# Performance work log

Measured on AMD Instinct MI355X. Metric: run time of the kernel, lower is better.

Reference implementation:

```python
import jax, jax.numpy as jnp
import numpy as np

HID = 256

def lstm_cell(x, h, c, Wih, Whh, bih, bhh):
    # PyTorch LSTM gate order: i, f, g, o
    g = x @ Wih.T + h @ Whh.T + bih + bhh
    i, f, gg, o = jnp.split(g, 4, axis=-1)
    c = jax.nn.sigmoid(f) * c + jax.nn.sigmoid(i) * jnp.tanh(gg)
    h = jax.nn.sigmoid(o) * jnp.tanh(c)
    return h, c

def lstm_seq(x, Wih, Whh, bih, bhh):
    # x: [B, T, D] -> outputs [B, T, H], final (h, c)
    B = x.shape[0]
    h0 = jnp.zeros((B, HID), x.dtype)
    def step(carry, xt):
        h, c = lstm_cell(xt, carry[0], carry[1], Wih, Whh, bih, bhh)
        return (h, c), h
    (h, c), ys = jax.lax.scan(step, (h0, h0), jnp.swapaxes(x, 0, 1))
    return jnp.swapaxes(ys, 0, 1), h, c

def setup_inputs():
    key = jax.random.key(0)
    B, M, H_WIN, NTH, NTW = 512, 16, 25, 64, 64
    SAL = NTH * NTW
    ks = iter(jax.random.split(key, 40))
    def U(shape):
        return jax.random.uniform(next(ks), shape, jnp.float32, -0.0625, 0.0625)
    def lstm_p(pfx, din):
        return {pfx + '_Wih': U((4 * HID, din)), pfx + '_Whh': U((4 * HID, HID)),
                pfx + '_bih': U((4 * HID,)), pfx + '_bhh': U((4 * HID,))}
    inp = {
        'encoder_position_inputs': jax.random.normal(next(ks), (B, M, 3), jnp.float32) * 0.1,
        'encoder_saliency_inputs': jax.random.uniform(next(ks), (B, M, NTH, NTW), jnp.float32),
        'decoder_position_inputs': jax.random.normal(next(ks), (B, 1, 3), jnp.float32) * 0.1,
        'decoder_saliency_inputs': jax.random.uniform(next(ks), (B, H_WIN, NTH, NTW), jnp.float32),
    }
    for pfx, din in [('pe', 3), ('se', SAL), ('fe', 2 * HID), ('pd', 3), ('sd', SAL), ('fd', 2 * HID)]:
        inp.update(lstm_p(pfx, din))
    inp['f2_W'] = U((HID, HID)); inp['f2_b'] = U((HID,))
    inp['out_W'] = U((3, HID)); inp['out_b'] = U((3,))
    return inp

def reference(encoder_position_inputs, encoder_saliency_inputs, decoder_position_inputs, decoder_saliency_inputs,
              pe_Wih, pe_Whh, pe_bih, pe_bhh, se_Wih, se_Whh, se_bih, se_bhh,
              fe_Wih, fe_Whh, fe_bih, fe_bhh, pd_Wih, pd_Whh, pd_bih, pd_bhh,
              sd_Wih, sd_Whh, sd_bih, sd_bhh, fd_Wih, fd_Whh, fd_bih, fd_bhh,
              f2_W, f2_b, out_W, out_b):
    B, M = encoder_position_inputs.shape[:2]
    SAL = encoder_saliency_inputs.shape[2] * encoder_saliency_inputs.shape[3]
    # encoder
    out_pos, h1, c1 = lstm_seq(encoder_position_inputs, pe_Wih, pe_Whh, pe_bih, pe_bhh)
    out_sal, h2, c2 = lstm_seq(encoder_saliency_inputs.reshape(B, M, SAL), se_Wih, se_Whh, se_bih, se_bhh)
    conc_enc = jnp.concatenate([out_sal, out_pos], axis=-1)
    _, hf, cf = lstm_seq(conc_enc, fe_Wih, fe_Whh, fe_bih, fe_bhh)
    # decoder: H_WINDOW single-step recurrence; fuse LSTM restarts from (hf, cf) every step
    dec_sal = decoder_saliency_inputs.reshape(B, -1, SAL)
    def step(carry, sal_t):
        inp, h1, c1, h2, c2 = carry
        h1, c1 = lstm_cell(inp, h1, c1, pd_Wih, pd_Whh, pd_bih, pd_bhh)
        h2, c2 = lstm_cell(sal_t, h2, c2, sd_Wih, sd_Whh, sd_bih, sd_bhh)
        conc = jnp.concatenate([h2, h1], axis=-1)
        hfd, _ = lstm_cell(conc, hf, cf, fd_Wih, fd_Whh, fd_bih, fd_bhh)
        fuse2 = hfd @ f2_W.T + f2_b
        delta = fuse2 @ out_W.T + out_b
        pred = inp + delta  # toPosition: orientation + motion
        return (pred, h1, c1, h2, c2), pred
    init = (decoder_position_inputs[:, 0], h1, c1, h2, c2)
    _, preds = jax.lax.scan(step, init, jnp.swapaxes(dec_sal, 0, 1))
    return jnp.swapaxes(preds, 0, 1)  # [B, H_WINDOW, 3]
```

## Files before the change

### kernel.cpp

```cpp
#include <hip/hip_runtime.h>

#define HID 256
#define BATCH 512
#define MENC 16
#define HWIN 25
#define SALSZ 4096
#define BH (BATCH * HID)

typedef __attribute__((ext_vector_type(8))) short bf16x8;
typedef __attribute__((ext_vector_type(4))) float f32x4;

__device__ __forceinline__ float sigmf(float x) { return 1.0f / (1.0f + __expf(-x)); }
__device__ __forceinline__ ushort f2bf(float f) {
    uint32_t u = __float_as_uint(f);
    return (ushort)((u + 0x7fffu + ((u >> 16) & 1u)) >> 16);
}

#define GLOAD_LDS(gp, lp) \
    __builtin_amdgcn_global_load_lds((const __attribute__((address_space(1))) void*)(gp), \
                                     (__attribute__((address_space(3))) void*)(lp), 16, 0, 0)

__device__ __forceinline__ void st_u64(void* p, unsigned long long v) {
    __hip_atomic_store((unsigned long long*)p, v, __ATOMIC_RELAXED, __HIP_MEMORY_SCOPE_AGENT);
}

__device__ __forceinline__ void gbar_arrive(unsigned int* slot)
{
    __syncthreads();
    if (threadIdx.x == 0) atomicAdd(slot, 1u);
}
__device__ __forceinline__ void gbar_wait(unsigned int* slot, unsigned int nblk)
{
    if (threadIdx.x == 0) {
        while (__hip_atomic_load(slot, __ATOMIC_RELAXED, __HIP_MEMORY_SCOPE_AGENT) < nblk)
            __builtin_amdgcn_s_sleep(1);
    }
    __syncthreads();
}

__device__ __forceinline__ void stage_wtile(const ushort* Wsrc, int ldw, int u0,
                                            ushort* lds, int lane, int wq)
{
    const int sub = lane >> 5, uu = lane & 31;
#pragma unroll
    for (int i = 0; i < 8; ++i) {
        const int row = i * 8 + wq * 2 + sub;
        const int su  = uu ^ (row & 7);
        const int gr  = (row >> 4) * HID + u0 + (row & 15);
        GLOAD_LDS(Wsrc + (size_t)gr * ldw + su * 8, lds + i * 2048 + wq * 512);
    }
}

__device__ __forceinline__ void cell_g(const ushort* hrow0, int ldh,
                                       const ushort* WsL, f32x4 acc[4], int lane)
{
    const int fr = lane & 15, fq = lane >> 4;
    const ushort* hrow = hrow0 + (size_t)fr * ldh;
#pragma unroll
    for (int ks = 0; ks < 8; ++ks) {
        const bf16x8 af = *(const bf16x8*)(hrow + ks * 32 + fq * 8);
#pragma unroll
        for (int g = 0; g < 4; ++g) {
            const int vr = g * 16 + fr;
            const bf16x8 bf = *(const bf16x8*)(WsL + vr * 256 + (((ks * 4 + fq)) ^ (vr & 7)) * 8);
            acc[g] = __builtin_amdgcn_mfma_f32_16x16x32_bf16(af, bf, acc[g], 0, 0, 0);
        }
    }
}

struct Cvt9 {
    const float* s[9];
    ushort*      d[9];
    int          end[9];
};
__global__ __launch_bounds__(256)
void cvt_multi(Cvt9 A)
{
    int i = blockIdx.x * 256 + threadIdx.x;
    if (i >= A.end[8]) return;
    int seg = 0, beg = 0;
#pragma unroll
    for (int k = 0; k < 8; ++k)
        if (i >= A.end[k]) { seg = k + 1; beg = A.end[k]; }
    const int j = i - beg;
    const float4 v = *(const float4*)(A.s[seg] + (size_t)j * 4);
    *(ushort4*)(A.d[seg] + (size_t)j * 4) = make_ushort4(f2bf(v.x), f2bf(v.y), f2bf(v.z), f2bf(v.w));
}

__device__ __forceinline__ void loadA128(const float* Ag, int lda, int tid, float4 ra[4])
{
#pragma unroll
    for (int j = 0; j < 2; ++j) {
        const int idx = j * 512 + tid;
        const int row = idx >> 3, u = idx & 7;
        const int su = (u ^ (row & 7)) * 8;
        ra[2 * j + 0] = *(const float4*)(Ag + (size_t)row * lda + su);
        ra[2 * j + 1] = *(const float4*)(Ag + (size_t)row * lda + su + 4);
    }
}
__device__ __forceinline__ void writeA128(const float4 ra[4], ushort* Al, int tid)
{
#pragma unroll
    for (int j = 0; j < 2; ++j) {
        const int idx = j * 512 + tid;
        uint4 v;
        v.x = (uint)f2bf(ra[2 * j].x) | ((uint)f2bf(ra[2 * j].y) << 16);
        v.y = (uint)f2bf(ra[2 * j].z) | ((uint)f2bf(ra[2 * j].w) << 16);
        v.z = (uint)f2bf(ra[2 * j + 1].x) | ((uint)f2bf(ra[2 * j + 1].y) << 16);
        v.w = (uint)f2bf(ra[2 * j + 1].z) | ((uint)f2bf(ra[2 * j + 1].w) << 16);
        *(uint4*)(Al + idx * 8) = v;
    }
}
__device__ __forceinline__ void stageB128(const ushort* Bg, int ldw, ushort* Bl, int tid)
{
#pragma unroll
    for (int j = 0; j < 2; ++j) {
        const int idx = j * 512 + tid;
        const int row = idx >> 3, u = idx & 7;
        const int su = (u ^ (row & 7)) * 8;
        GLOAD_LDS(Bg + (size_t)row * ldw + su, Bl + idx * 8);
    }
}

__global__ __launch_bounds__(512, 4)
void gemm128f(const float* __restrict__ A, const ushort* __restrict__ W,
              float* __restrict__ C, int M, int N, int K,
              int lda, int ldw, int ldc)
{
    __shared__ ushort As[2][128 * 64];
    __shared__ ushort Bs[2][128 * 64];
    const int tid = threadIdx.x, lane = tid & 63, wid = tid >> 6;

    const int gx = gridDim.x, nwg = gx * gridDim.y;
    int bid = blockIdx.y * gx + blockIdx.x;
    {
        const int q = nwg >> 3, r = nwg & 7;
        const int xcd = bid & 7, o = bid >> 3;
        bid = (xcd < r) ? xcd * (q + 1) + o : r * (q + 1) + (xcd - r) * q + o;
    }
    const int m0 = (bid / gx) * 128, n0 = (bid % gx) * 128;

    const int wr = wid >> 1, wc = wid & 1;
    const int fr = lane & 15, fq = lane >> 4;

    f32x4 acc[2][4] = {};
    const int nt = K / 64;
    const float*  Ab0 = A + (size_t)m0 * lda;
    const ushort* Bb0 = W + (size_t)n0 * ldw;

    float4 ra[4];
    loadA128(Ab0, lda, tid, ra);
    stageB128(Bb0, ldw, Bs[0], tid);
    writeA128(ra, As[0], tid);
    loadA128(Ab0 + 64, lda, tid, ra);
    asm volatile("s_waitcnt vmcnt(4) lgkmcnt(0)" ::: "memory");
    __builtin_amdgcn_sched_barrier(0);
    __builtin_amdgcn_s_barrier();
    __builtin_amdgcn_sched_barrier(0);

    for (int t = 0; t < nt; ++t) {
        const int p = t & 1;
        const int t1 = (t + 1 < nt) ? t + 1 : nt - 1;
        const int t2 = (t + 2 < nt) ? t + 2 : nt - 1;
        stageB128(Bb0 + t1 * 64, ldw, Bs[p ^ 1], tid);
        writeA128(ra, As[p ^ 1], tid);
        loadA128(Ab0 + t2 * 64, lda, tid, ra);

        const ushort* Ab = As[p];
        const ushort* Bb = Bs[p];
#pragma unroll
        for (int ks = 0; ks < 2; ++ks) {
            bf16x8 bfr[4];
#pragma unroll
            for (int nf = 0; nf < 4; ++nf) {
                const int row = wc * 64 + nf * 16 + fr;
                bfr[nf] = *(const bf16x8*)(Bb + row * 64 + ((ks * 4 + fq) ^ (row & 7)) * 8);
            }
            bf16x8 af[2];
#pragma unroll
            for (int mf = 0; mf < 2; ++mf) {
                const int row = wr * 32 + mf * 16 + fr;
                af[mf] = *(const bf16x8*)(Ab + row * 64 + ((ks * 4 + fq) ^ (row & 7)) * 8);
            }
            __builtin_amdgcn_s_setprio(1);
#pragma unroll
            for (int mf = 0; mf < 2; ++mf)
#pragma unroll
                for (int nf = 0; nf < 4; ++nf)
                    acc[mf][nf] = __builtin_amdgcn_mfma_f32_16x16x32_bf16(
                        af[mf], bfr[nf], acc[mf][nf], 0, 0, 0);
            __builtin_amdgcn_s_setprio(0);
        }
        if (t == nt - 1) break;
        asm volatile("s_waitcnt vmcnt(4) lgkmcnt(0)" ::: "memory");
        __builtin_amdgcn_sched_barrier(0);
        __builtin_amdgcn_s_barrier();
        __builtin_amdgcn_sched_barrier(0);
    }

    const int cl = lane & 15, ch = lane >> 4;
#pragma unroll
    for (int mf = 0; mf < 2; ++mf)
#pragma unroll
        for (int nf = 0; nf < 4; ++nf)
#pragma unroll
            for (int r = 0; r < 4; ++r)
                C[(size_t)(m0 + wr * 32 + mf * 16 + ch * 4 + r) * ldc
                  + n0 + wc * 64 + nf * 16 + cl] = acc[mf][nf][r];
}

__global__ __launch_bounds__(256)
void gemm_mfma_bt(const ushort* __restrict__ A, const ushort* __restrict__ W,
                  float* __restrict__ C, int M, int N, int K,
                  int lda, int ldw, int ldc, const float* __restrict__ rbias)
{
    __shared__ ushort As[128 * 32];
    __shared__ ushort Bs[128 * 32];
    const int t    = threadIdx.x;
    const int lane = t & 63, wid = t >> 6;
    const int m0 = blockIdx.y * 128, n0 = blockIdx.x * 128;
    const int wr = wid >> 1, wc = wid & 1;

    f32x4 acc[4][4] = {};

    const int sr = wid * 16 + (lane >> 2);
    const int su = ((lane & 3) ^ ((lane >> 3) & 3)) * 8;
    const ushort* Ag = A + (size_t)(m0 + sr) * lda + su;
    const ushort* Wg = W + (size_t)(n0 + sr) * ldw + su;
    ushort* Al = As + wid * 512;
    ushort* Bl = Bs + wid * 512;

    const int fr = lane & 15;
    const int fq = lane >> 4;
    const int sw = (fr >> 1) & 3;

    for (int k0 = 0; k0 < K; k0 += 32) {
        GLOAD_LDS(Ag,                    Al);
        GLOAD_LDS(Ag + (size_t)64 * lda, Al + 2048);
        GLOAD_LDS(Wg,                    Bl);
        GLOAD_LDS(Wg + (size_t)64 * ldw, Bl + 2048);
        Ag += 32; Wg += 32;
        __syncthreads();

        bf16x8 af[4], bfr[4];
#pragma unroll
        for (int m = 0; m < 4; ++m)
            af[m] = *(const bf16x8*)(As + (wr * 64 + m * 16 + fr) * 32 + (fq ^ sw) * 8);
#pragma unroll
        for (int n = 0; n < 4; ++n)
            bfr[n] = *(const bf16x8*)(Bs + (wc * 64 + n * 16 + fr) * 32 + (fq ^ sw) * 8);
#pragma unroll
        for (int m = 0; m < 4; ++m)
#pragma unroll
            for (int n = 0; n < 4; ++n)
                acc[m][n] = __builtin_amdgcn_mfma_f32_16x16x32_bf16(af[m], bfr[n], acc[m][n], 0, 0, 0);
        __syncthreads();
    }

    const int cl = lane & 15, ch = lane >> 4;
#pragma unroll
    for (int m = 0; m < 4; ++m)
#pragma unroll
        for (int n = 0; n < 4; ++n)
#pragma unroll
            for (int r = 0; r < 4; ++r) {
                const int mm = m0 + wr * 64 + m * 16 + ch * 4 + r;
                const int nn = n0 + wc * 64 + n * 16 + cl;
                float v = acc[m][n][r];
                if (rbias) v += rbias[(size_t)(mm & 511) * ldc + nn];
                C[(size_t)mm * ldc + nn] = v;
            }
}

__global__ __launch_bounds__(256)
void gemm_tn(const float* __restrict__ A, const float* __restrict__ W,
             const float* __restrict__ b1, const float* __restrict__ b2,
             float* __restrict__ C,
             int M, int N, int K, int lda, int ldw, int ldc)
{
    __shared__ float AsT[16][68];
    __shared__ float WsT[16][68];
    const int t  = threadIdx.x;
    const int tx = t & 15, ty = t >> 4;
    const int m0 = blockIdx.y * 64, n0 = blockIdx.x * 64;
    const int lr = t >> 2;
    const int c4 = t & 3;

    float acc[4][4];
#pragma unroll
    for (int i = 0; i < 4; ++i)
#pragma unroll
        for (int j = 0; j < 4; ++j) acc[i][j] = 0.0f;

    for (int k0 = 0; k0 < K; k0 += 16) {
        float a[4], w[4];
        const int kb = k0 + c4 * 4;
#pragma unroll
        for (int k = 0; k < 4; ++k) {
            a[k] = (kb + k < K) ? A[(size_t)(m0 + lr) * lda + kb + k] : 0.0f;
            w[k] = (kb + k < K) ? W[(size_t)(n0 + lr) * ldw + kb + k] : 0.0f;
        }
        __syncthreads();
#pragma unroll
        for (int k = 0; k < 4; ++k) {
            AsT[c4 * 4 + k][lr] = a[k];
            WsT[c4 * 4 + k][lr] = w[k];
        }
        __syncthreads();
#pragma unroll
        for (int kk = 0; kk < 16; ++kk) {
            const float4 av = *(const float4*)&AsT[kk][ty * 4];
            const float4 wv = *(const float4*)&WsT[kk][tx * 4];
            acc[0][0] += av.x * wv.x; acc[0][1] += av.x * wv.y; acc[0][2] += av.x * wv.z; acc[0][3] += av.x * wv.w;
            acc[1][0] += av.y * wv.x; acc[1][1] += av.y * wv.y; acc[1][2] += av.y * wv.z; acc[1][3] += av.y * wv.w;
            acc[2][0] += av.z * wv.x; acc[2][1] += av.z * wv.y; acc[2][2] += av.z * wv.z; acc[2][3] += av.z * wv.w;
            acc[3][0] += av.w * wv.x; acc[3][1] += av.w * wv.y; acc[3][2] += av.w * wv.z; acc[3][3] += av.w * wv.w;
        }
    }

#pragma unroll
    for (int i = 0; i < 4; ++i) {
        const int m = m0 + ty * 4 + i;
#pragma unroll
        for (int j = 0; j < 4; ++j) {
            const int n = n0 + tx * 4 + j;
            float v = acc[i][j];
            if (b1) v += b1[n];
            if (b2) v += b2[n];
            C[(size_t)m * ldc + n] = v;
        }
    }
}

struct EncArgs {
    const ushort *WHse, *WHpe;
    const float  *xg_se;
    const float  *enc_pos;
    const float  *se_b1, *se_b2, *pe_b1, *pe_b2;
    const float  *pe_Wih;
    ushort       *conc;
    float        *SE_C, *PE_C;
    unsigned int *bar;
};

__global__ __launch_bounds__(1024)
void enc_chain(EncArgs A)
{
    __shared__ ushort Ws[4][64 * 256];
    __shared__ ushort hloc[64][64];
    const int tid = threadIdx.x, lane = tid & 63, w = tid >> 6;
    const int role  = blockIdx.x >> 5;
    const int rem   = blockIdx.x & 31;
    const int btile = rem & 7, usup = rem >> 3;
    const int b0 = btile * 64, ub = usup * 64;
    const int usub = w & 3, bsub = w >> 2;
    const int u0t = ub + usub * 16;
    const int grp = role * 8 + btile;
    const int fr = lane & 15, fq = lane >> 4;
    const int u = u0t + fr;
    const int ul = usub * 16 + fr;
    const int coff = role ? 256 : 0;

    stage_wtile(role ? A.WHpe : A.WHse, HID, u0t, Ws[usub], lane, bsub);

    const float* b1 = role ? A.pe_b1 : A.se_b1;
    const float* b2 = role ? A.pe_b2 : A.se_b2;
    float bias[4], wxs[4][3];
#pragma unroll
    for (int g = 0; g < 4; ++g) {
        bias[g] = b1[g * HID + u] + b2[g * HID + u];
        wxs[g][0] = wxs[g][1] = wxs[g][2] = 0.0f;
        if (role) {
            wxs[g][0] = A.pe_Wih[(g * HID + u) * 3 + 0];
            wxs[g][1] = A.pe_Wih[(g * HID + u) * 3 + 1];
            wxs[g][2] = A.pe_Wih[(g * HID + u) * 3 + 2];
        }
    }
    float c[4] = {0.f, 0.f, 0.f, 0.f};
    __syncthreads();

    for (int t = 0; t < MENC; ++t) {
        float xg[4][4];
#pragma unroll
        for (int r = 0; r < 4; ++r) {
            const int b = b0 + bsub * 16 + fq * 4 + r;
            if (role) {
                const float* xp = A.enc_pos + ((size_t)b * MENC + t) * 3;
                xg[r][0] = xp[0]; xg[r][1] = xp[1]; xg[r][2] = xp[2]; xg[r][3] = 0.f;
            } else {
#pragma unroll
                for (int g = 0; g < 4; ++g)
                    xg[r][g] = A.xg_se[((size_t)b * MENC + t) * 1024 + g * HID + u];
            }
        }
        if (t > 0) gbar_wait(A.bar + grp * MENC + (t - 1), 4);
        f32x4 acc[4] = {};
        if (t > 0)
            cell_g(A.conc + ((size_t)(t - 1) * 512 + b0 + bsub * 16) * 512 + coff, 512,
                   Ws[usub], acc, lane);
#pragma unroll
        for (int r = 0; r < 4; ++r) {
            const int bl = bsub * 16 + fq * 4 + r;
            const int b = b0 + bl;
            float gv[4];
#pragma unroll
            for (int g = 0; g < 4; ++g) {
                float v = acc[g][r] + bias[g];
                if (role) v += xg[r][0] * wxs[g][0] + xg[r][1] * wxs[g][1] + xg[r][2] * wxs[g][2];
                else      v += xg[r][g];
                gv[g] = v;
            }
            const float cn = sigmf(gv[1]) * c[r] + sigmf(gv[0]) * tanhf(gv[2]);
            const float hn = sigmf(gv[3]) * tanhf(cn);
            c[r] = cn;
            hloc[bl][ul] = f2bf(hn);
            if (t == MENC - 1) (role ? A.PE_C : A.SE_C)[(size_t)b * HID + u] = cn;
        }
        __syncthreads();
        {
            const int row = tid >> 4, c8 = tid & 15;
            const unsigned long long v = *(const unsigned long long*)&hloc[row][c8 * 4];
            st_u64(A.conc + ((size_t)t * 512 + b0 + row) * 512 + coff + ub + c8 * 4, v);
        }
        if (t != MENC - 1) gbar_arrive(A.bar + grp * MENC + t);
    }
}

struct MidArgs {
    const ushort *WHsd, *WHfe;
    const float  *xg_sd;
    const float  *xg_fe;
    const float  *sd_b1, *sd_b2, *fe_b1, *fe_b2;
    const ushort *conc;
    const float  *SE_C;
    ushort       *SDB;
    ushort       *FEB;
    float        *FEH, *FE_C;
    unsigned int *bar;
};

__global__ __launch_bounds__(1024)
void mid_chain(MidArgs A)
{
    __shared__ ushort Ws[4][64 * 256];
    __shared__ ushort hloc[64][64];
    const int tid = threadIdx.x, lane = tid & 63, w = tid >> 6;
    const int role  = blockIdx.x >> 5;
    const int rem   = blockIdx.x & 31;
    const int btile = rem & 7, usup = rem >> 3;
    const int b0 = btile * 64, ub = usup * 64;
    const int usub = w & 3, bsub = w >> 2;
    const int u0t = ub + usub * 16;
    const int grp = role * 8 + btile;
    const int fr = lane & 15, fq = lane >> 4;
    const int u = u0t + fr;
    const int ul = usub * 16 + fr;
    const int NT = role ? MENC : HWIN;

    stage_wtile(role ? A.WHfe : A.WHsd, HID, u0t, Ws[usub], lane, bsub);

    const float* b1 = role ? A.fe_b1 : A.sd_b1;
    const float* b2 = role ? A.fe_b2 : A.sd_b2;
    float bias[4];
#pragma unroll
    for (int g = 0; g < 4; ++g) bias[g] = b1[g * HID + u] + b2[g * HID + u];

    float c[4];
#pragma unroll
    for (int r = 0; r < 4; ++r) {
        const int b = b0 + bsub * 16 + fq * 4 + r;
        c[r] = role ? 0.0f : A.SE_C[(size_t)b * HID + u];
    }
    __syncthreads();

    for (int t = 0; t < NT; ++t) {
        float xg[4][4];
#pragma unroll
        for (int r = 0; r < 4; ++r) {
            const int b = b0 + bsub * 16 + fq * 4 + r;
#pragma unroll
            for (int g = 0; g < 4; ++g)
                xg[r][g] = role ? A.xg_fe[((size_t)t * 512 + b) * 1024 + g * HID + u]
                                : A.xg_sd[((size_t)b * HWIN + t) * 1024 + g * HID + u];
        }
        if (t > 0) gbar_wait(A.bar + grp * HWIN + (t - 1), 4);
        f32x4 acc[4] = {};
        if (role == 0) {
            if (t == 0) cell_g(A.conc + ((size_t)15 * 512 + b0 + bsub * 16) * 512, 512,
                               Ws[usub], acc, lane);
            else        cell_g(A.SDB + ((size_t)(t - 1) * 512 + b0 + bsub * 16) * HID, HID,
                               Ws[usub], acc, lane);
        } else if (t > 0) {
            cell_g(A.FEB + ((size_t)(t - 1) * BATCH + b0 + bsub * 16) * HID, HID,
                   Ws[usub], acc, lane);
        }
#pragma unroll
        for (int r = 0; r < 4; ++r) {
            const int bl = bsub * 16 + fq * 4 + r;
            const int b = b0 + bl;
            float gv[4];
#pragma unroll
            for (int g = 0; g < 4; ++g)
                gv[g] = acc[g][r] + bias[g] + xg[r][g];
            const float cn = sigmf(gv[1]) * c[r] + sigmf(gv[0]) * tanhf(gv[2]);
            const float hn = sigmf(gv[3]) * tanhf(cn);
            c[r] = cn;
            hloc[bl][ul] = f2bf(hn);
            if (role == 1 && t == MENC - 1) {
                A.FEH[(size_t)b * HID + u] = hn;
                A.FE_C[(size_t)b * HID + u] = cn;
            }
        }
        __syncthreads();
        {
            const int row = tid >> 4, c8 = tid & 15;
            const unsigned long long v = *(const unsigned long long*)&hloc[row][c8 * 4];
            ushort* dst = role ? (A.FEB + ((size_t)t * BATCH + b0 + row) * 256 + ub + c8 * 4)
                               : (A.SDB + ((size_t)t * 512 + b0 + row) * 256 + ub + c8 * 4);
            st_u64(dst, v);
        }
        if (t != NT - 1) gbar_arrive(A.bar + grp * HWIN + t);
    }
}

struct DecArgs {
    const ushort *WHpd;
    const ushort *WFDh;
    const ushort *peF;
    const float  *PE_C, *FE_C;
    const float  *xh2;
    const float  *pd_b1, *pd_b2, *pd_Wih;
    const float  *G, *c3, *dec_pos;
    ushort       *H1;
    float        *DELTA;
    float        *out;
    unsigned int *bar;
};

__global__ __launch_bounds__(512)
void dec_chain(DecArgs A)
{
    __shared__ ushort Wpd[2][64 * 256], Wfd[2][64 * 256];
    __shared__ ushort hloc[64][32];
    __shared__ float pred_lds[192];
    const int tid = threadIdx.x, lane = tid & 63, w = tid >> 6;
    const int btile = blockIdx.x & 7, usup = blockIdx.x >> 3;
    const int b0 = btile * 64, ub = usup * 32;
    const int usub = w & 1, bsub = w >> 1;
    const int u0t = ub + usub * 16;
    const int fr = lane & 15, fq = lane >> 4;
    const int u = u0t + fr;
    const int ul = usub * 16 + fr;
    unsigned int* bars = A.bar + btile * 2 * HWIN;

    stage_wtile(A.WHpd, HID, u0t, Wpd[usub], lane, bsub);
    stage_wtile(A.WFDh, 512, u0t, Wfd[usub], lane, bsub);

    float pdb[4], wxs[4][3], cf[4], c1[4], Gu[3];
#pragma unroll
    for (int g = 0; g < 4; ++g) {
        pdb[g] = A.pd_b1[g * HID + u] + A.pd_b2[g * HID + u];
        wxs[g][0] = A.pd_Wih[(g * HID + u) * 3 + 0];
        wxs[g][1] = A.pd_Wih[(g * HID + u) * 3 + 1];
        wxs[g][2] = A.pd_Wih[(g * HID + u) * 3 + 2];
    }
#pragma unroll
    for (int r = 0; r < 4; ++r) {
        const int b = b0 + bsub * 16 + fq * 4 + r;
        c1[r] = A.PE_C[(size_t)b * HID + u];
        cf[r] = A.FE_C[(size_t)b * HID + u];
    }
    Gu[0] = A.G[0 * HID + u]; Gu[1] = A.G[1 * HID + u]; Gu[2] = A.G[2 * HID + u];
    const float c3r = (tid < 192) ? A.c3[tid % 3] : 0.0f;
    if (tid < 192) pred_lds[tid] = A.dec_pos[(size_t)(b0 + tid / 3) * 3 + tid % 3];
    __syncthreads();

    for (int t = 0; t < HWIN; ++t) {
        f32x4 acc[4] = {};
        if (t == 0) cell_g(A.peF + (size_t)(b0 + bsub * 16) * 512, 512, Wpd[usub], acc, lane);
        else        cell_g(A.H1 + ((size_t)(t - 1) * BATCH + b0 + bsub * 16) * HID, HID,
                           Wpd[usub], acc, lane);
        if (t > 0) {
            gbar_wait(bars + 2 * (t - 1) + 1, 8);
            if (tid < 192) {
                pred_lds[tid] += A.DELTA[((size_t)(t - 1) * 512 + b0 + tid / 3) * 3 + tid % 3] + c3r;
                if (usup == 0)
                    A.out[((size_t)(b0 + tid / 3) * HWIN + (t - 1)) * 3 + tid % 3] = pred_lds[tid];
            }
            __syncthreads();
        }
#pragma unroll
        for (int r = 0; r < 4; ++r) {
            const int bl = bsub * 16 + fq * 4 + r;
            const float x0 = pred_lds[bl * 3 + 0];
            const float x1 = pred_lds[bl * 3 + 1];
            const float x2 = pred_lds[bl * 3 + 2];
            float gv[4];
#pragma unroll
            for (int g = 0; g < 4; ++g)
                gv[g] = acc[g][r] + pdb[g] + x0 * wxs[g][0] + x1 * wxs[g][1] + x2 * wxs[g][2];
            const float cn = sigmf(gv[1]) * c1[r] + sigmf(gv[0]) * tanhf(gv[2]);
            const float hn = sigmf(gv[3]) * tanhf(cn);
            c1[r] = cn;
            hloc[bl][ul] = f2bf(hn);
        }
        __syncthreads();
        {
            const int row = tid >> 3, c8 = tid & 7;
            const unsigned long long v = *(const unsigned long long*)&hloc[row][c8 * 4];
            st_u64(A.H1 + ((size_t)t * BATCH + b0 + row) * 256 + ub + c8 * 4, v);
        }
        gbar_arrive(bars + 2 * t);
        float xh[4][4];
#pragma unroll
        for (int r = 0; r < 4; ++r) {
            const int b = b0 + bsub * 16 + fq * 4 + r;
#pragma unroll
            for (int g = 0; g < 4; ++g)
                xh[r][g] = A.xh2[((size_t)t * 512 + b) * 1024 + g * HID + u];
        }
        gbar_wait(bars + 2 * t, 8);
        {
            f32x4 accB[4] = {};
            cell_g(A.H1 + ((size_t)t * BATCH + b0 + bsub * 16) * HID, HID,
                   Wfd[usub], accB, lane);
#pragma unroll
            for (int r = 0; r < 4; ++r) {
                const int b = b0 + bsub * 16 + fq * 4 + r;
                float gv[4];
#pragma unroll
                for (int g = 0; g < 4; ++g)
                    gv[g] = accB[g][r] + xh[r][g];
                const float cn = sigmf(gv[1]) * cf[r] + sigmf(gv[0]) * tanhf(gv[2]);
                const float hn = sigmf(gv[3]) * tanhf(cn);
                float p0 = hn * Gu[0], p1 = hn * Gu[1], p2 = hn * Gu[2];
#pragma unroll
                for (int s = 1; s < 16; s <<= 1) {
                    p0 += __shfl_xor(p0, s);
                    p1 += __shfl_xor(p1, s);
                    p2 += __shfl_xor(p2, s);
                }
                if (fr == 0) {
                    float* d = A.DELTA + ((size_t)t * 512 + b) * 3;
                    atomicAdd(d + 0, p0); atomicAdd(d + 1, p1); atomicAdd(d + 2, p2);
                }
            }
        }
        gbar_arrive(bars + 2 * t + 1);
    }
    gbar_wait(bars + 2 * (HWIN - 1) + 1, 8);
    if (tid < 192) {
        pred_lds[tid] += A.DELTA[((size_t)(HWIN - 1) * 512 + b0 + tid / 3) * 3 + tid % 3] + c3r;
        if (usup == 0)
            A.out[((size_t)(b0 + tid / 3) * HWIN + (HWIN - 1)) * 3 + tid % 3] = pred_lds[tid];
    }
}

__global__ __launch_bounds__(256)
void precompute_G(const float* __restrict__ f2W, const float* __restrict__ f2b,
                  const float* __restrict__ outW, const float* __restrict__ outb,
                  float* __restrict__ G, float* __restrict__ c3)
{
    const int k = threadIdx.x;
    float g0 = 0.f, g1 = 0.f, g2 = 0.f;
    for (int n = 0; n < HID; ++n) {
        const float w = f2W[n * HID + k];
        g0 += outW[n] * w;
        g1 += outW[HID + n] * w;
        g2 += outW[2 * HID + n] * w;
    }
    G[k] = g0; G[HID + k] = g1; G[2 * HID + k] = g2;
    if (k < 3) {
        float s = outb[k];
        for (int n = 0; n < HID; ++n) s += outW[k * HID + n] * f2b[n];
        c3[k] = s;
    }
}

extern "C" void kernel_launch(void* const* d_in, const int* in_sizes, int n_in,
                              void* d_out, int out_size, void* d_ws, size_t ws_size,
                              hipStream_t stream)
{
    (void)in_sizes; (void)n_in; (void)out_size; (void)ws_size;
    const float* enc_pos = (const float*)d_in[0];
    const float* enc_sal = (const float*)d_in[1];
    const float* dec_pos = (const float*)d_in[2];
    const float* dec_sal = (const float*)d_in[3];
    const float *pe_Wih = (const float*)d_in[4],  *pe_Whh = (const float*)d_in[5],
                *pe_bih = (const float*)d_in[6],  *pe_bhh = (const float*)d_in[7];
    const float *se_Wih = (const float*)d_in[8],  *se_Whh = (const float*)d_in[9],
                *se_bih = (const float*)d_in[10], *se_bhh = (const float*)d_in[11];
    const float *fe_Wih = (const float*)d_in[12], *fe_Whh = (const float*)d_in[13],
                *fe_bih = (const float*)d_in[14], *fe_bhh = (const float*)d_in[15];
    const float *pd_Wih = (const float*)d_in[16], *pd_Whh = (const float*)d_in[17],
                *pd_bih = (const float*)d_in[18], *pd_bhh = (const float*)d_in[19];
    const float *sd_Wih = (const float*)d_in[20], *sd_Whh = (const float*)d_in[21],
                *sd_bih = (const float*)d_in[22], *sd_bhh = (const float*)d_in[23];
    const float *fd_Wih = (const float*)d_in[24], *fd_Whh = (const float*)d_in[25],
                *fd_bih = (const float*)d_in[26], *fd_bhh = (const float*)d_in[27];
    const float *f2_W = (const float*)d_in[28], *f2_b = (const float*)d_in[29];
    const float *out_W = (const float*)d_in[30], *out_b = (const float*)d_in[31];
    float* out = (float*)d_out;
    float* ws  = (float*)d_ws;

    size_t off = 0;
    float* XG_SE = ws + off; off += (size_t)8192 * 1024;
    float* XG_FE = ws + off; off += (size_t)8192 * 1024;
    float* BIG   = ws + off; off += (size_t)12800 * 1024;
    float* BIG2  = ws + off; off += (size_t)12800 * 1024;
    float* GBIAS = ws + off; off += (size_t)BATCH * 1024;
    float* PE_C  = ws + off; off += BH;
    float* SE_C  = ws + off; off += BH;
    float* FE_C  = ws + off; off += BH;
    float* FEH   = ws + off; off += BH;
    float* Gm    = ws + off; off += 1024;
    float* C3    = ws + off; off += 8;
    float* DELTA = ws + off; off += (size_t)HWIN * BATCH * 3 + 64;
    unsigned int* BAR = (unsigned int*)(ws + off); off += 1280;
    ushort* WSE  = (ushort*)(ws + off); off += ((size_t)1024 * 4096) / 2;
    ushort* WSD  = (ushort*)(ws + off); off += ((size_t)1024 * 4096) / 2;
    ushort* WFE  = (ushort*)(ws + off); off += ((size_t)1024 * 512) / 2;
    ushort* WFD  = (ushort*)(ws + off); off += ((size_t)1024 * 512) / 2;
    ushort* WHpe = (ushort*)(ws + off); off += ((size_t)1024 * 256) / 2;
    ushort* WHse = (ushort*)(ws + off); off += ((size_t)1024 * 256) / 2;
    ushort* WHfe = (ushort*)(ws + off); off += ((size_t)1024 * 256) / 2;
    ushort* WHsd = (ushort*)(ws + off); off += ((size_t)1024 * 256) / 2;
    ushort* WHpd = (ushort*)(ws + off); off += ((size_t)1024 * 256) / 2;
    ushort* CONC = (ushort*)(ws + off); off += ((size_t)MENC * 512 * 512) / 2;
    ushort* SDB  = (ushort*)(ws + off); off += ((size_t)HWIN * BH) / 2;
    ushort* FEB  = (ushort*)(ws + off); off += ((size_t)MENC * BH) / 2;
    ushort* H1   = (ushort*)(ws + off); off += ((size_t)HWIN * BH) / 2;

    hipMemsetAsync(DELTA, 0, ((size_t)HWIN * BATCH * 3 + 64 + 1280) * 4, stream);

    auto mgemm = [&](const ushort* A, const ushort* W, float* C,
                     int M, int N, int K, int lda, int ldw, int ldc, const float* rb) {
        gemm_mfma_bt<<<dim3(N / 128, M / 128), 256, 0, stream>>>(A, W, C, M, N, K, lda, ldw, ldc, rb);
    };
    auto mgemm128f = [&](const float* A, const ushort* W, float* C,
                         int M, int N, int K, int lda, int ldw, int ldc) {
        gemm128f<<<dim3(N / 128, M / 128), 512, 0, stream>>>(A, W, C, M, N, K, lda, ldw, ldc);
    };

    {
        Cvt9 a;
        const float* srcs[9] = { se_Wih, sd_Wih, fe_Wih, fd_Wih, pe_Whh, se_Whh, fe_Whh, sd_Whh, pd_Whh };
        ushort*      dsts[9] = { WSE,    WSD,    WFE,    WFD,    WHpe,   WHse,   WHfe,   WHsd,   WHpd };
        const int    n4s[9]  = { 1024*4096/4, 1024*4096/4, 1024*512/4, 1024*512/4,
                                 1024*256/4, 1024*256/4, 1024*256/4, 1024*256/4, 1024*256/4 };
        int acc9 = 0;
        for (int i = 0; i < 9; ++i) { a.s[i] = srcs[i]; a.d[i] = dsts[i]; acc9 += n4s[i]; a.end[i] = acc9; }
        cvt_multi<<<(acc9 + 255) / 256, 256, 0, stream>>>(a);
    }
    precompute_G<<<1, 256, 0, stream>>>(f2_W, f2_b, out_W, out_b, Gm, C3);

    mgemm128f(enc_sal, WSE, XG_SE, 8192, 1024, SALSZ, SALSZ, SALSZ, 1024);
    mgemm128f(dec_sal, WSD, BIG, 12800, 1024, SALSZ, SALSZ, SALSZ, 1024);

    {
        EncArgs a;
        a.WHse = WHse; a.WHpe = WHpe; a.xg_se = XG_SE; a.enc_pos = enc_pos;
        a.se_b1 = se_bih; a.se_b2 = se_bhh; a.pe_b1 = pe_bih; a.pe_b2 = pe_bhh;
        a.pe_Wih = pe_Wih; a.conc = CONC; a.SE_C = SE_C; a.PE_C = PE_C;
        a.bar = BAR;
        enc_chain<<<64, 1024, 0, stream>>>(a);
    }

    mgemm(CONC, WFE, XG_FE, 8192, 1024, 512, 512, 512, 1024, nullptr);

    {
        MidArgs a;
        a.WHsd = WHsd; a.WHfe = WHfe; a.xg_sd = BIG; a.xg_fe = XG_FE;
        a.sd_b1 = sd_bih; a.sd_b2 = sd_bhh; a.fe_b1 = fe_bih; a.fe_b2 = fe_bhh;
        a.conc = CONC; a.SE_C = SE_C; a.SDB = SDB; a.FEB = FEB;
        a.FEH = FEH; a.FE_C = FE_C; a.bar = BAR + 256;
        mid_chain<<<64, 1024, 0, stream>>>(a);
    }

    gemm_tn<<<dim3(16, 8), 256, 0, stream>>>(FEH, fd_Whh, fd_bih, fd_bhh, GBIAS,
                                             BATCH, 1024, HID, HID, HID, 1024);
    mgemm(SDB, WFD, BIG2, 12800, 1024, HID, HID, 512, 1024, GBIAS);

    {
        DecArgs a;
        a.WHpd = WHpd; a.WFDh = WFD + 256;
        a.peF = CONC + ((size_t)15 * 512) * 512 + 256;
        a.PE_C = PE_C; a.FE_C = FE_C; a.xh2 = BIG2;
        a.pd_b1 = pd_bih; a.pd_b2 = pd_bhh; a.pd_Wih = pd_Wih;
        a.G = Gm; a.c3 = C3; a.dec_pos = dec_pos;
        a.H1 = H1; a.DELTA = DELTA; a.out = out; a.bar = BAR + 656;
        dec_chain<<<64, 512, 0, stream>>>(a);
    }
}
```

Measured before the change: 1.145 ms.

## Overlap decoder saliency GEMM with encoder recurrence in one fused launch

Merges the decoder saliency input GEMM into the encoder recurrence kernel. Blocks 0-127 run the encoder LSTM chain, now spread over 128 blocks of 512 threads instead of 64 of 1024, and the remaining 800 blocks run the 128x128 GEMM tiles. The goal is to keep most CUs busy with GEMM work while the latency-bound recurrence runs on only a few. The risk is a deadlock or slowdown if the chain blocks, which spin on grid barriers, are not all resident together, and GEMM blocks may compete with them for bandwidth.

```diff
diff --git a/kernel.cpp b/kernel.cpp
--- a/kernel.cpp
+++ b/kernel.cpp
@@ -122,17 +122,12 @@
     }
 }
 
-__global__ __launch_bounds__(512, 4)
-void gemm128f(const float* __restrict__ A, const ushort* __restrict__ W,
-              float* __restrict__ C, int M, int N, int K,
-              int lda, int ldw, int ldc)
-{
-    __shared__ ushort As[2][128 * 64];
-    __shared__ ushort Bs[2][128 * 64];
-    const int tid = threadIdx.x, lane = tid & 63, wid = tid >> 6;
-
-    const int gx = gridDim.x, nwg = gx * gridDim.y;
-    int bid = blockIdx.y * gx + blockIdx.x;
+__device__ __forceinline__ void gemm128f_body(
+    const float* __restrict__ A, const ushort* __restrict__ W, float* __restrict__ C,
+    int lda, int ldw, int ldc, int K, int gx, int nwg, int bid,
+    ushort* AsB, ushort* BsB, int tid)
+{
+    const int lane = tid & 63, wid = tid >> 6;
     {
         const int q = nwg >> 3, r = nwg & 7;
         const int xcd = bid & 7, o = bid >> 3;
@@ -150,8 +145,8 @@
 
     float4 ra[4];
     loadA128(Ab0, lda, tid, ra);
-    stageB128(Bb0, ldw, Bs[0], tid);
-    writeA128(ra, As[0], tid);
+    stageB128(Bb0, ldw, BsB, tid);
+    writeA128(ra, AsB, tid);
     loadA128(Ab0 + 64, lda, tid, ra);
     asm volatile("s_waitcnt vmcnt(4) lgkmcnt(0)" ::: "memory");
     __builtin_amdgcn_sched_barrier(0);
@@ -162,12 +157,12 @@
         const int p = t & 1;
         const int t1 = (t + 1 < nt) ? t + 1 : nt - 1;
         const int t2 = (t + 2 < nt) ? t + 2 : nt - 1;
-        stageB128(Bb0 + t1 * 64, ldw, Bs[p ^ 1], tid);
-        writeA128(ra, As[p ^ 1], tid);
+        stageB128(Bb0 + t1 * 64, ldw, BsB + (p ^ 1) * 8192, tid);
+        writeA128(ra, AsB + (p ^ 1) * 8192, tid);
         loadA128(Ab0 + t2 * 64, lda, tid, ra);
 
-        const ushort* Ab = As[p];
-        const ushort* Bb = Bs[p];
+        const ushort* Ab = AsB + p * 8192;
+        const ushort* Bb = BsB + p * 8192;
 #pragma unroll
         for (int ks = 0; ks < 2; ++ks) {
             bf16x8 bfr[4];
@@ -209,127 +204,13 @@
                   + n0 + wc * 64 + nf * 16 + cl] = acc[mf][nf][r];
 }
 
-__global__ __launch_bounds__(256)
-void gemm_mfma_bt(const ushort* __restrict__ A, const ushort* __restrict__ W,
-                  float* __restrict__ C, int M, int N, int K,
-                  int lda, int ldw, int ldc, const float* __restrict__ rbias)
-{
-    __shared__ ushort As[128 * 32];
-    __shared__ ushort Bs[128 * 32];
-    const int t    = threadIdx.x;
-    const int lane = t & 63, wid = t >> 6;
-    const int m0 = blockIdx.y * 128, n0 = blockIdx.x * 128;
-    const int wr = wid >> 1, wc = wid & 1;
-
-    f32x4 acc[4][4] = {};
-
-    const int sr = wid * 16 + (lane >> 2);
-    const int su = ((lane & 3) ^ ((lane >> 3) & 3)) * 8;
-    const ushort* Ag = A + (size_t)(m0 + sr) * lda + su;
-    const ushort* Wg = W + (size_t)(n0 + sr) * ldw + su;
-    ushort* Al = As + wid * 512;
-    ushort* Bl = Bs + wid * 512;
-
-    const int fr = lane & 15;
-    const int fq = lane >> 4;
-    const int sw = (fr >> 1) & 3;
-
-    for (int k0 = 0; k0 < K; k0 += 32) {
-        GLOAD_LDS(Ag,                    Al);
-        GLOAD_LDS(Ag + (size_t)64 * lda, Al + 2048);
-        GLOAD_LDS(Wg,                    Bl);
-        GLOAD_LDS(Wg + (size_t)64 * ldw, Bl + 2048);
-        Ag += 32; Wg += 32;
-        __syncthreads();
-
-        bf16x8 af[4], bfr[4];
-#pragma unroll
-        for (int m = 0; m < 4; ++m)
-            af[m] = *(const bf16x8*)(As + (wr * 64 + m * 16 + fr) * 32 + (fq ^ sw) * 8);
-#pragma unroll
-        for (int n = 0; n < 4; ++n)
-            bfr[n] = *(const bf16x8*)(Bs + (wc * 64 + n * 16 + fr) * 32 + (fq ^ sw) * 8);
-#pragma unroll
-        for (int m = 0; m < 4; ++m)
-#pragma unroll
-            for (int n = 0; n < 4; ++n)
-                acc[m][n] = __builtin_amdgcn_mfma_f32_16x16x32_bf16(af[m], bfr[n], acc[m][n], 0, 0, 0);
-        __syncthreads();
-    }
-
-    const int cl = lane & 15, ch = lane >> 4;
-#pragma unroll
-    for (int m = 0; m < 4; ++m)
-#pragma unroll
-        for (int n = 0; n < 4; ++n)
-#pragma unroll
-            for (int r = 0; r < 4; ++r) {
-                const int mm = m0 + wr * 64 + m * 16 + ch * 4 + r;
-                const int nn = n0 + wc * 64 + n * 16 + cl;
-                float v = acc[m][n][r];
-                if (rbias) v += rbias[(size_t)(mm & 511) * ldc + nn];
-                C[(size_t)mm * ldc + nn] = v;
-            }
-}
-
-__global__ __launch_bounds__(256)
-void gemm_tn(const float* __restrict__ A, const float* __restrict__ W,
-             const float* __restrict__ b1, const float* __restrict__ b2,
-             float* __restrict__ C,
-             int M, int N, int K, int lda, int ldw, int ldc)
-{
-    __shared__ float AsT[16][68];
-    __shared__ float WsT[16][68];
-    const int t  = threadIdx.x;
-    const int tx = t & 15, ty = t >> 4;
-    const int m0 = blockIdx.y * 64, n0 = blockIdx.x * 64;
-    const int lr = t >> 2;
-    const int c4 = t & 3;
-
-    float acc[4][4];
-#pragma unroll
-    for (int i = 0; i < 4; ++i)
-#pragma unroll
-        for (int j = 0; j < 4; ++j) acc[i][j] = 0.0f;
-
-    for (int k0 = 0; k0 < K; k0 += 16) {
-        float a[4], w[4];
-        const int kb = k0 + c4 * 4;
-#pragma unroll
-        for (int k = 0; k < 4; ++k) {
-            a[k] = (kb + k < K) ? A[(size_t)(m0 + lr) * lda + kb + k] : 0.0f;
-            w[k] = (kb + k < K) ? W[(size_t)(n0 + lr) * ldw + kb + k] : 0.0f;
-        }
-        __syncthreads();
-#pragma unroll
-        for (int k = 0; k < 4; ++k) {
-            AsT[c4 * 4 + k][lr] = a[k];
-            WsT[c4 * 4 + k][lr] = w[k];
-        }
-        __syncthreads();
-#pragma unroll
-        for (int kk = 0; kk < 16; ++kk) {
-            const float4 av = *(const float4*)&AsT[kk][ty * 4];
-            const float4 wv = *(const float4*)&WsT[kk][tx * 4];
-            acc[0][0] += av.x * wv.x; acc[0][1] += av.x * wv.y; acc[0][2] += av.x * wv.z; acc[0][3] += av.x * wv.w;
-            acc[1][0] += av.y * wv.x; acc[1][1] += av.y * wv.y; acc[1][2] += av.y * wv.z; acc[1][3] += av.y * wv.w;
-            acc[2][0] += av.z * wv.x; acc[2][1] += av.z * wv.y; acc[2][2] += av.z * wv.z; acc[2][3] += av.z * wv.w;
-            acc[3][0] += av.w * wv.x; acc[3][1] += av.w * wv.y; acc[3][2] += av.w * wv.z; acc[3][3] += av.w * wv.w;
-        }
-    }
-
-#pragma unroll
-    for (int i = 0; i < 4; ++i) {
-        const int m = m0 + ty * 4 + i;
-#pragma unroll
-        for (int j = 0; j < 4; ++j) {
-            const int n = n0 + tx * 4 + j;
-            float v = acc[i][j];
-            if (b1) v += b1[n];
-            if (b2) v += b2[n];
-            C[(size_t)m * ldc + n] = v;
-        }
-    }
+__global__ __launch_bounds__(512, 4)
+void gemm128f(const float* __restrict__ A, const ushort* __restrict__ W,
+              float* __restrict__ C, int gx, int nwg)
+{
+    __shared__ ushort As[2 * 128 * 64];
+    __shared__ ushort Bs[2 * 128 * 64];
+    gemm128f_body(A, W, C, SALSZ, SALSZ, 1024, SALSZ, gx, nwg, blockIdx.x, As, Bs, threadIdx.x);
 }
 
 struct EncArgs {
@@ -343,25 +224,35 @@
     unsigned int *bar;
 };
 
-__global__ __launch_bounds__(1024)
-void enc_chain(EncArgs A)
-{
-    __shared__ ushort Ws[4][64 * 256];
-    __shared__ ushort hloc[64][64];
-    const int tid = threadIdx.x, lane = tid & 63, w = tid >> 6;
-    const int role  = blockIdx.x >> 5;
-    const int rem   = blockIdx.x & 31;
+__global__ __launch_bounds__(512, 4)
+void enc_sd(EncArgs A, const float* __restrict__ sdA, const ushort* __restrict__ sdW,
+            float* __restrict__ sdC)
+{
+    __shared__ ushort sh[34816];
+    const int tid = threadIdx.x;
+
+    if (blockIdx.x >= 128) {
+        gemm128f_body(sdA, sdW, sdC, SALSZ, SALSZ, 1024, SALSZ, 8, 800,
+                      (int)blockIdx.x - 128, sh, sh + 16384, tid);
+        return;
+    }
+
+    const int lane = tid & 63, w = tid >> 6;
+    const int role  = blockIdx.x >> 6;
+    const int rem   = blockIdx.x & 63;
     const int btile = rem & 7, usup = rem >> 3;
-    const int b0 = btile * 64, ub = usup * 64;
-    const int usub = w & 3, bsub = w >> 2;
+    const int b0 = btile * 64, ub = usup * 32;
+    const int usub = w & 1, bsub = w >> 1;
     const int u0t = ub + usub * 16;
     const int grp = role * 8 + btile;
     const int fr = lane & 15, fq = lane >> 4;
     const int u = u0t + fr;
     const int ul = usub * 16 + fr;
     const int coff = role ? 256 : 0;
-
-    stage_wtile(role ? A.WHpe : A.WHse, HID, u0t, Ws[usub], lane, bsub);
+    ushort* Ws0 = sh + usub * 16384;
+    ushort (*hloc)[32] = (ushort(*)[32])(sh + 32768);
+
+    stage_wtile(role ? A.WHpe : A.WHse, HID, u0t, Ws0, lane, bsub);
 
     const float* b1 = role ? A.pe_b1 : A.se_b1;
     const float* b2 = role ? A.pe_b2 : A.se_b2;
@@ -393,11 +284,11 @@
                     xg[r][g] = A.xg_se[((size_t)b * MENC + t) * 1024 + g * HID + u];
             }
         }
-        if (t > 0) gbar_wait(A.bar + grp * MENC + (t - 1), 4);
+        if (t > 0) gbar_wait(A.bar + grp * MENC + (t - 1), 8);
         f32x4 acc[4] = {};
         if (t > 0)
             cell_g(A.conc + ((size_t)(t - 1) * 512 + b0 + bsub * 16) * 512 + coff, 512,
-                   Ws[usub], acc, lane);
+                   Ws0, acc, lane);
 #pragma unroll
         for (int r = 0; r < 4; ++r) {
             const int bl = bsub * 16 + fq * 4 + r;
@@ -418,11 +309,134 @@
         }
         __syncthreads();
         {
-            const int row = tid >> 4, c8 = tid & 15;
+            const int row = tid >> 3, c8 = tid & 7;
             const unsigned long long v = *(const unsigned long long*)&hloc[row][c8 * 4];
             st_u64(A.conc + ((size_t)t * 512 + b0 + row) * 512 + coff + ub + c8 * 4, v);
         }
         if (t != MENC - 1) gbar_arrive(A.bar + grp * MENC + t);
+    }
+}
+
+__global__ __launch_bounds__(256)
+void gemm_mfma_bt(const ushort* __restrict__ A, const ushort* __restrict__ W,
+                  float* __restrict__ C, int M, int N, int K,
+                  int lda, int ldw, int ldc, const float* __restrict__ rbias)
+{
+    __shared__ ushort As[128 * 32];
+    __shared__ ushort Bs[128 * 32];
+    const int t    = threadIdx.x;
+    const int lane = t & 63, wid = t >> 6;
+    const int m0 = blockIdx.y * 128, n0 = blockIdx.x * 128;
+    const int wr = wid >> 1, wc = wid & 1;
+
+    f32x4 acc[4][4] = {};
+
+    const int sr = wid * 16 + (lane >> 2);
+    const int su = ((lane & 3) ^ ((lane >> 3) & 3)) * 8;
+    const ushort* Ag = A + (size_t)(m0 + sr) * lda + su;
+    const ushort* Wg = W + (size_t)(n0 + sr) * ldw + su;
+    ushort* Al = As + wid * 512;
+    ushort* Bl = Bs + wid * 512;
+
+    const int fr = lane & 15;
+    const int fq = lane >> 4;
+    const int sw = (fr >> 1) & 3;
+
+    for (int k0 = 0; k0 < K; k0 += 32) {
+        GLOAD_LDS(Ag,                    Al);
+        GLOAD_LDS(Ag + (size_t)64 * lda, Al + 2048);
+        GLOAD_LDS(Wg,                    Bl);
+        GLOAD_LDS(Wg + (size_t)64 * ldw, Bl + 2048);
+        Ag += 32; Wg += 32;
+        __syncthreads();
+
+        bf16x8 af[4], bfr[4];
+#pragma unroll
+        for (int m = 0; m < 4; ++m)
+            af[m] = *(const bf16x8*)(As + (wr * 64 + m * 16 + fr) * 32 + (fq ^ sw) * 8);
+#pragma unroll
+        for (int n = 0; n < 4; ++n)
+            bfr[n] = *(const bf16x8*)(Bs + (wc * 64 + n * 16 + fr) * 32 + (fq ^ sw) * 8);
+#pragma unroll
+        for (int m = 0; m < 4; ++m)
+#pragma unroll
+            for (int n = 0; n < 4; ++n)
+                acc[m][n] = __builtin_amdgcn_mfma_f32_16x16x32_bf16(af[m], bfr[n], acc[m][n], 0, 0, 0);
+        __syncthreads();
+    }
+
+    const int cl = lane & 15, ch = lane >> 4;
+#pragma unroll
+    for (int m = 0; m < 4; ++m)
+#pragma unroll
+        for (int n = 0; n < 4; ++n)
+#pragma unroll
+            for (int r = 0; r < 4; ++r) {
+                const int mm = m0 + wr * 64 + m * 16 + ch * 4 + r;
+                const int nn = n0 + wc * 64 + n * 16 + cl;
+                float v = acc[m][n][r];
+                if (rbias) v += rbias[(size_t)(mm & 511) * ldc + nn];
+                C[(size_t)mm * ldc + nn] = v;
+            }
+}
+
+__global__ __launch_bounds__(256)
+void gemm_tn(const float* __restrict__ A, const float* __restrict__ W,
+             const float* __restrict__ b1, const float* __restrict__ b2,
+             float* __restrict__ C,
+             int M, int N, int K, int lda, int ldw, int ldc)
+{
+    __shared__ float AsT[16][68];
+    __shared__ float WsT[16][68];
+    const int t  = threadIdx.x;
+    const int tx = t & 15, ty = t >> 4;
+    const int m0 = blockIdx.y * 64, n0 = blockIdx.x * 64;
+    const int lr = t >> 2;
+    const int c4 = t & 3;
+
+    float acc[4][4];
+#pragma unroll
+    for (int i = 0; i < 4; ++i)
+#pragma unroll
+        for (int j = 0; j < 4; ++j) acc[i][j] = 0.0f;
+
+    for (int k0 = 0; k0 < K; k0 += 16) {
+        float a[4], w[4];
+        const int kb = k0 + c4 * 4;
+#pragma unroll
+        for (int k = 0; k < 4; ++k) {
+            a[k] = (kb + k < K) ? A[(size_t)(m0 + lr) * lda + kb + k] : 0.0f;
+            w[k] = (kb + k < K) ? W[(size_t)(n0 + lr) * ldw + kb + k] : 0.0f;
+        }
+        __syncthreads();
+#pragma unroll
+        for (int k = 0; k < 4; ++k) {
+            AsT[c4 * 4 + k][lr] = a[k];
+            WsT[c4 * 4 + k][lr] = w[k];
+        }
+        __syncthreads();
+#pragma unroll
+        for (int kk = 0; kk < 16; ++kk) {
+            const float4 av = *(const float4*)&AsT[kk][ty * 4];
+            const float4 wv = *(const float4*)&WsT[kk][tx * 4];
+            acc[0][0] += av.x * wv.x; acc[0][1] += av.x * wv.y; acc[0][2] += av.x * wv.z; acc[0][3] += av.x * wv.w;
+            acc[1][0] += av.y * wv.x; acc[1][1] += av.y * wv.y; acc[1][2] += av.y * wv.z; acc[1][3] += av.y * wv.w;
+            acc[2][0] += av.z * wv.x; acc[2][1] += av.z * wv.y; acc[2][2] += av.z * wv.z; acc[2][3] += av.z * wv.w;
+            acc[3][0] += av.w * wv.x; acc[3][1] += av.w * wv.y; acc[3][2] += av.w * wv.z; acc[3][3] += av.w * wv.w;
+        }
+    }
+
+#pragma unroll
+    for (int i = 0; i < 4; ++i) {
+        const int m = m0 + ty * 4 + i;
+#pragma unroll
+        for (int j = 0; j < 4; ++j) {
+            const int n = n0 + tx * 4 + j;
+            float v = acc[i][j];
+            if (b1) v += b1[n];
+            if (b2) v += b2[n];
+            C[(size_t)m * ldc + n] = v;
+        }
     }
 }
 
@@ -737,10 +751,6 @@
                      int M, int N, int K, int lda, int ldw, int ldc, const float* rb) {
         gemm_mfma_bt<<<dim3(N / 128, M / 128), 256, 0, stream>>>(A, W, C, M, N, K, lda, ldw, ldc, rb);
     };
-    auto mgemm128f = [&](const float* A, const ushort* W, float* C,
-                         int M, int N, int K, int lda, int ldw, int ldc) {
-        gemm128f<<<dim3(N / 128, M / 128), 512, 0, stream>>>(A, W, C, M, N, K, lda, ldw, ldc);
-    };
 
     {
         Cvt9 a;
@@ -754,8 +764,7 @@
     }
     precompute_G<<<1, 256, 0, stream>>>(f2_W, f2_b, out_W, out_b, Gm, C3);
 
-    mgemm128f(enc_sal, WSE, XG_SE, 8192, 1024, SALSZ, SALSZ, SALSZ, 1024);
-    mgemm128f(dec_sal, WSD, BIG, 12800, 1024, SALSZ, SALSZ, SALSZ, 1024);
+    gemm128f<<<512, 512, 0, stream>>>(enc_sal, WSE, XG_SE, 8, 512);
 
     {
         EncArgs a;
@@ -763,7 +772,7 @@
         a.se_b1 = se_bih; a.se_b2 = se_bhh; a.pe_b1 = pe_bih; a.pe_b2 = pe_bhh;
         a.pe_Wih = pe_Wih; a.conc = CONC; a.SE_C = SE_C; a.PE_C = PE_C;
         a.bar = BAR;
-        enc_chain<<<64, 1024, 0, stream>>>(a);
+        enc_sd<<<928, 512, 0, stream>>>(a, dec_sal, WSD, BIG);
     }
 
     mgemm(CONC, WFE, XG_FE, 8192, 1024, 512, 512, 512, 1024, nullptr);
```

Result: faster. 1.033 ms (-9.8%).
